# Optimization experiments

Hardware: AMD Instinct MI355X
Metric: run time of the kernel (lower is better)

The kernel has to match this reference:

```python
import jax, jax.numpy as jnp
import numpy as np

M = 128  # split point: first M units use max-plus, rest use min-plus

def setup_inputs() -> dict:
    key = jax.random.key(0)
    k1, k2 = jax.random.split(key)
    x = jax.random.normal(k1, (2048, 512), dtype=jnp.float32)   # (batch, features_in)
    w = jax.random.normal(k2, (512, 256), dtype=jnp.float32)    # (features_in, units)
    return {"x": x, "w": w}

def reference(x, w):
    # Tropical (max/min-plus) pseudo-matmul.
    # s[b, f, u] = x[b, f] + w[f, u]; reduce over f.
    s_max = x[:, :, None] + w[None, :, :M]          # (batch, f, M)
    s_min = x[:, :, None] + w[None, :, M:]          # (batch, f, units-M)
    hv = jnp.max(s_max, axis=1)                     # (batch, M)
    hw = jnp.min(s_min, axis=1)                     # (batch, units-M)
    return jnp.concatenate([hv, hw], axis=1)        # linear activation = identity
```

## Files before the change

kernel.cpp:

```cpp
#include <hip/hip_runtime.h>
#include <math.h>


#define FEAT  512
#define UNITS 256
#define BR    8
#define KW    64
#define NW    8
#define NQ    (KW / 4)

__device__ __forceinline__ float max3(float a, float b, float c) {
    return fmaxf(fmaxf(a, b), c);
}

__device__ __forceinline__ void load_xquad(const float* __restrict__ lds, int kb, int q,
                                           float4* __restrict__ xb) {
    #pragma unroll
    for (int r = 0; r < BR; ++r)
        xb[r] = *(const float4*)&lds[r * FEAT + kb + q * 4];
}

__device__ __forceinline__ void load_wquad(const float* __restrict__ wp, int q,
                                           float4* __restrict__ wb) {
    #pragma unroll
    for (int k = 0; k < 4; ++k)
        wb[k] = *(const float4*)(wp + (size_t)(q * 4 + k) * UNITS);
}

__device__ __forceinline__ void compute_quad(const float4* __restrict__ xb,
                                             const float4* __restrict__ wq,
                                             float sgn, float4* __restrict__ acc) {
    const float4 w0 = make_float4(wq[0].x*sgn, wq[0].y*sgn, wq[0].z*sgn, wq[0].w*sgn);
    const float4 w1 = make_float4(wq[1].x*sgn, wq[1].y*sgn, wq[1].z*sgn, wq[1].w*sgn);
    const float4 w2 = make_float4(wq[2].x*sgn, wq[2].y*sgn, wq[2].z*sgn, wq[2].w*sgn);
    const float4 w3 = make_float4(wq[3].x*sgn, wq[3].y*sgn, wq[3].z*sgn, wq[3].w*sgn);
    #pragma unroll
    for (int r = 0; r < BR; ++r) {
        const float4 a = xb[r];
        float4 A = acc[r];
        A.x = max3(A.x, fmaf(a.x, sgn, w0.x), fmaf(a.y, sgn, w1.x));
        A.x = max3(A.x, fmaf(a.z, sgn, w2.x), fmaf(a.w, sgn, w3.x));
        A.y = max3(A.y, fmaf(a.x, sgn, w0.y), fmaf(a.y, sgn, w1.y));
        A.y = max3(A.y, fmaf(a.z, sgn, w2.y), fmaf(a.w, sgn, w3.y));
        A.z = max3(A.z, fmaf(a.x, sgn, w0.z), fmaf(a.y, sgn, w1.z));
        A.z = max3(A.z, fmaf(a.z, sgn, w2.z), fmaf(a.w, sgn, w3.z));
        A.w = max3(A.w, fmaf(a.x, sgn, w0.w), fmaf(a.y, sgn, w1.w));
        A.w = max3(A.w, fmaf(a.z, sgn, w2.w), fmaf(a.w, sgn, w3.w));
        acc[r] = A;
    }
}

__global__ __launch_bounds__(512) void tropical_kernel(const float* __restrict__ x,
                                                       const float* __restrict__ w,
                                                       float* __restrict__ out) {
    __shared__ float lds[NW * BR * UNITS];
    const int tid  = threadIdx.x;
    const int lane = tid & 63;
    const int wv   = __builtin_amdgcn_readfirstlane(tid >> 6);
    const int u0   = lane * 4;
    const float sgn = (lane < 32) ? 1.0f : -1.0f;
    const int row0 = blockIdx.x * BR;
    const int kb   = wv * KW;

    {
        const float4* src = (const float4*)(x + (size_t)row0 * FEAT);
        ((float4*)lds)[tid]       = src[tid];
        ((float4*)lds)[tid + 512] = src[tid + 512];
    }

    const float* wp = w + (size_t)kb * UNITS + u0;

    float4 acc[BR];
    #pragma unroll
    for (int r = 0; r < BR; ++r)
        acc[r] = make_float4(-__builtin_inff(), -__builtin_inff(),
                             -__builtin_inff(), -__builtin_inff());

    float4 xA[BR], xB[BR], wA[4], wB[4];
    load_wquad(wp, 0, wA);

    __syncthreads();
    load_xquad(lds, kb, 0, xA);

    #pragma unroll 1
    for (int q = 0; q < NQ; q += 2) {
        load_wquad(wp, q + 1, wB);
        load_xquad(lds, kb, q + 1, xB);
        compute_quad(xA, wA, sgn, acc);
        if (q + 2 < NQ) {
            load_wquad(wp, q + 2, wA);
            load_xquad(lds, kb, q + 2, xA);
        }
        compute_quad(xB, wB, sgn, acc);
    }

    __syncthreads();
    #pragma unroll
    for (int r = 0; r < BR; ++r)
        *(float4*)&lds[((wv * BR + r) * UNITS) + u0] = acc[r];
    __syncthreads();

    const int r  = tid >> 6;
    const int uo = (tid & 63) * 4;
    float4 v = *(const float4*)&lds[(0 * BR + r) * UNITS + uo];
    #pragma unroll
    for (int j = 1; j < NW; ++j) {
        const float4 p = *(const float4*)&lds[(j * BR + r) * UNITS + uo];
        v.x = fmaxf(v.x, p.x);
        v.y = fmaxf(v.y, p.y);
        v.z = fmaxf(v.z, p.z);
        v.w = fmaxf(v.w, p.w);
    }
    const float so = (uo < 128) ? 1.0f : -1.0f;
    *(float4*)&out[(size_t)(row0 + r) * UNITS + uo] =
        make_float4(v.x * so, v.y * so, v.z * so, v.w * so);
}

extern "C" void kernel_launch(void* const* d_in, const int* in_sizes, int n_in,
                              void* d_out, int out_size, void* d_ws, size_t ws_size,
                              hipStream_t stream) {
    const float* x = (const float*)d_in[0];
    const float* w = (const float*)d_in[1];
    float* out = (float*)d_out;

    tropical_kernel<<<dim3(2048 / BR), dim3(512), 0, stream>>>(x, w, out);
}
```

Before: 67.70 us.

## Use packed v2f FMA/max ops and separate LDS partial buffer to drop a barrier

Rewrites the inner tropical accumulation to use two-wide packed float FMA and max operations, with the weight sign applied once at load time. It also gives the x tile and the partial-result scratch separate LDS regions, which removes the barrier before the partials are written. The goal is fewer VALU instructions per update on hardware with packed FP32 math, plus one less block-wide sync. The risks are that the compiler splits the packed ops back into scalar ones, and that the larger LDS footprint limits occupancy.

```diff
diff --git a/kernel.cpp b/kernel.cpp
--- a/kernel.cpp
+++ b/kernel.cpp
@@ -8,57 +8,67 @@
 #define KW    64
 #define NW    8
 #define NQ    (KW / 4)
+#define PART  4096
 
-__device__ __forceinline__ float max3(float a, float b, float c) {
-    return fmaxf(fmaxf(a, b), c);
+typedef float v2f __attribute__((ext_vector_type(2)));
+
+__device__ __forceinline__ v2f pk_max(v2f a, v2f b) {
+    return __builtin_elementwise_max(a, b);
+}
+__device__ __forceinline__ v2f pk_fma(v2f a, v2f b, v2f c) {
+    return __builtin_elementwise_fma(a, b, c);
 }
 
-__device__ __forceinline__ void load_xquad(const float* __restrict__ lds, int kb, int q,
-                                           float4* __restrict__ xb) {
+__device__ __forceinline__ void load_xquad(const float* __restrict__ lds,
+                                           int kb, int q, float4* __restrict__ xb) {
     #pragma unroll
     for (int r = 0; r < BR; ++r)
         xb[r] = *(const float4*)&lds[r * FEAT + kb + q * 4];
 }
 
-__device__ __forceinline__ void load_wquad(const float* __restrict__ wp, int q,
-                                           float4* __restrict__ wb) {
+__device__ __forceinline__ void load_wquad_sgn(const float* __restrict__ wp, int q,
+                                               v2f sgn2, v2f* __restrict__ wsg) {
     #pragma unroll
-    for (int k = 0; k < 4; ++k)
-        wb[k] = *(const float4*)(wp + (size_t)(q * 4 + k) * UNITS);
+    for (int k = 0; k < 4; ++k) {
+        const float4 wk = *(const float4*)(wp + (size_t)(q * 4 + k) * UNITS);
+        wsg[2 * k + 0] = v2f{wk.x, wk.y} * sgn2;
+        wsg[2 * k + 1] = v2f{wk.z, wk.w} * sgn2;
+    }
 }
 
 __device__ __forceinline__ void compute_quad(const float4* __restrict__ xb,
-                                             const float4* __restrict__ wq,
-                                             float sgn, float4* __restrict__ acc) {
-    const float4 w0 = make_float4(wq[0].x*sgn, wq[0].y*sgn, wq[0].z*sgn, wq[0].w*sgn);
-    const float4 w1 = make_float4(wq[1].x*sgn, wq[1].y*sgn, wq[1].z*sgn, wq[1].w*sgn);
-    const float4 w2 = make_float4(wq[2].x*sgn, wq[2].y*sgn, wq[2].z*sgn, wq[2].w*sgn);
-    const float4 w3 = make_float4(wq[3].x*sgn, wq[3].y*sgn, wq[3].z*sgn, wq[3].w*sgn);
+                                             const v2f* __restrict__ wsg,
+                                             v2f sgn2, v2f (*__restrict__ acc)[2]) {
     #pragma unroll
     for (int r = 0; r < BR; ++r) {
         const float4 a = xb[r];
-        float4 A = acc[r];
-        A.x = max3(A.x, fmaf(a.x, sgn, w0.x), fmaf(a.y, sgn, w1.x));
-        A.x = max3(A.x, fmaf(a.z, sgn, w2.x), fmaf(a.w, sgn, w3.x));
-        A.y = max3(A.y, fmaf(a.x, sgn, w0.y), fmaf(a.y, sgn, w1.y));
-        A.y = max3(A.y, fmaf(a.z, sgn, w2.y), fmaf(a.w, sgn, w3.y));
-        A.z = max3(A.z, fmaf(a.x, sgn, w0.z), fmaf(a.y, sgn, w1.z));
-        A.z = max3(A.z, fmaf(a.z, sgn, w2.z), fmaf(a.w, sgn, w3.z));
-        A.w = max3(A.w, fmaf(a.x, sgn, w0.w), fmaf(a.y, sgn, w1.w));
-        A.w = max3(A.w, fmaf(a.z, sgn, w2.w), fmaf(a.w, sgn, w3.w));
-        acc[r] = A;
+        const v2f a0 = {a.x, a.x};
+        const v2f a1 = {a.y, a.y};
+        const v2f a2 = {a.z, a.z};
+        const v2f a3 = {a.w, a.w};
+        const v2f s0 = pk_fma(a0, sgn2, wsg[0]);
+        const v2f t0 = pk_fma(a0, sgn2, wsg[1]);
+        const v2f s1 = pk_fma(a1, sgn2, wsg[2]);
+        const v2f t1 = pk_fma(a1, sgn2, wsg[3]);
+        const v2f s2 = pk_fma(a2, sgn2, wsg[4]);
+        const v2f t2 = pk_fma(a2, sgn2, wsg[5]);
+        const v2f s3 = pk_fma(a3, sgn2, wsg[6]);
+        const v2f t3 = pk_fma(a3, sgn2, wsg[7]);
+        acc[r][0] = pk_max(acc[r][0], pk_max(pk_max(s0, s1), pk_max(s2, s3)));
+        acc[r][1] = pk_max(acc[r][1], pk_max(pk_max(t0, t1), pk_max(t2, t3)));
     }
 }
 
 __global__ __launch_bounds__(512) void tropical_kernel(const float* __restrict__ x,
                                                        const float* __restrict__ w,
                                                        float* __restrict__ out) {
-    __shared__ float lds[NW * BR * UNITS];
+    __shared__ float lds[PART + NW * BR * UNITS];
     const int tid  = threadIdx.x;
     const int lane = tid & 63;
     const int wv   = __builtin_amdgcn_readfirstlane(tid >> 6);
     const int u0   = lane * 4;
     const float sgn = (lane < 32) ? 1.0f : -1.0f;
+    const v2f  sgn2 = {sgn, sgn};
     const int row0 = blockIdx.x * BR;
     const int kb   = wv * KW;
 
@@ -70,42 +80,44 @@
 
     const float* wp = w + (size_t)kb * UNITS + u0;
 
-    float4 acc[BR];
+    v2f acc[BR][2];
     #pragma unroll
-    for (int r = 0; r < BR; ++r)
-        acc[r] = make_float4(-__builtin_inff(), -__builtin_inff(),
-                             -__builtin_inff(), -__builtin_inff());
+    for (int r = 0; r < BR; ++r) {
+        acc[r][0] = v2f{-__builtin_inff(), -__builtin_inff()};
+        acc[r][1] = v2f{-__builtin_inff(), -__builtin_inff()};
+    }
 
-    float4 xA[BR], xB[BR], wA[4], wB[4];
-    load_wquad(wp, 0, wA);
+    float4 xA[BR], xB[BR];
+    v2f wA[8], wB[8];
+    load_wquad_sgn(wp, 0, sgn2, wA);
 
     __syncthreads();
     load_xquad(lds, kb, 0, xA);
 
     #pragma unroll 1
     for (int q = 0; q < NQ; q += 2) {
-        load_wquad(wp, q + 1, wB);
+        load_wquad_sgn(wp, q + 1, sgn2, wB);
         load_xquad(lds, kb, q + 1, xB);
-        compute_quad(xA, wA, sgn, acc);
+        compute_quad(xA, wA, sgn2, acc);
         if (q + 2 < NQ) {
-            load_wquad(wp, q + 2, wA);
+            load_wquad_sgn(wp, q + 2, sgn2, wA);
             load_xquad(lds, kb, q + 2, xA);
         }
-        compute_quad(xB, wB, sgn, acc);
+        compute_quad(xB, wB, sgn2, acc);
     }
 
-    __syncthreads();
     #pragma unroll
     for (int r = 0; r < BR; ++r)
-        *(float4*)&lds[((wv * BR + r) * UNITS) + u0] = acc[r];
+        *(float4*)&lds[PART + ((wv * BR + r) * UNITS) + u0] =
+            make_float4(acc[r][0].x, acc[r][0].y, acc[r][1].x, acc[r][1].y);
     __syncthreads();
 
     const int r  = tid >> 6;
     const int uo = (tid & 63) * 4;
-    float4 v = *(const float4*)&lds[(0 * BR + r) * UNITS + uo];
+    float4 v = *(const float4*)&lds[PART + (0 * BR + r) * UNITS + uo];
     #pragma unroll
     for (int j = 1; j < NW; ++j) {
-        const float4 p = *(const float4*)&lds[(j * BR + r) * UNITS + uo];
+        const float4 p = *(const float4*)&lds[PART + (j * BR + r) * UNITS + uo];
         v.x = fmaxf(v.x, p.x);
         v.y = fmaxf(v.y, p.y);
         v.z = fmaxf(v.z, p.z);
```

Result: slower. 72.26 us (+6.7%).
